# Performance work log

Measured on AMD Instinct MI355X. Metric: run time of the kernel, lower is better.

## Reference

```python
import jax, jax.numpy as jnp
import numpy as np

N_HEADS = 16
NEG = -1e9  # matches torch masked_fill value


def setup_inputs() -> dict:
    key = jax.random.key(0)
    ks = jax.random.split(key, 8)
    B, S, E = 4, 1024, 1024
    x = jax.random.normal(ks[0], (B, S, E), dtype=jnp.float32)
    event_lengths = jax.random.randint(ks[1], (B,), 1, S + 1)
    scale = 1.0 / np.sqrt(E)
    Wq = jax.random.normal(ks[2], (E, E), dtype=jnp.float32) * scale
    bq = jnp.zeros((E,), dtype=jnp.float32)
    Wk = jax.random.normal(ks[3], (E, E), dtype=jnp.float32) * scale
    bk = jnp.zeros((E,), dtype=jnp.float32)
    Wv = jax.random.normal(ks[4], (E, E), dtype=jnp.float32) * scale
    bv = jnp.zeros((E,), dtype=jnp.float32)
    return {"x": x, "Wq": Wq, "bq": bq, "Wk": Wk, "bk": bk,
            "Wv": Wv, "bv": bv, "event_lengths": event_lengths}


def reference(x, Wq, bq, Wk, bk, Wv, bv, event_lengths):
    B, S, E = x.shape
    H = N_HEADS
    D = E // H
    # fused projections, then split heads: [B,S,E] -> [B,H,S,D]
    def split(t):
        return t.reshape(B, S, H, D).transpose(0, 2, 1, 3)
    q = split(x @ Wq + bq)
    k = split(x @ Wk + bk)
    v = split(x @ Wv + bv)
    scores = jnp.einsum('bhsd,bhtd->bhst', q, k) / jnp.sqrt(jnp.float32(D))
    # rectangular length mask: valid iff row < len AND col < len
    idx = jnp.arange(S)
    valid = idx[None, :] < event_lengths[:, None]           # [B,S]
    mask = valid[:, :, None] & valid[:, None, :]            # [B,S,S]
    scores = jnp.where(mask[:, None, :, :], scores, NEG)
    attn = jax.nn.softmax(scores, axis=-1)
    out = jnp.einsum('bhst,bhtd->bhsd', attn, v)            # [B,H,S,D]
    # concat heads (== torch.cat over head outputs); NOTE: summarize proj is
    # dead code in the original (its result is overwritten), dropout is eval-identity
    return out.transpose(0, 2, 1, 3).reshape(B, S, E)
```

## Files before the change

kernel.cpp:

```cpp
#include <hip/hip_runtime.h>
#include <stdint.h>


using u16     = unsigned short;
using half8   = __attribute__((ext_vector_type(8))) _Float16;
using floatx4 = __attribute__((ext_vector_type(4))) float;

#define MFMA16(a, b, c) __builtin_amdgcn_mfma_f32_16x16x32_f16(a, b, c, 0, 0, 0)

__device__ __forceinline__ u16 f2h(float f) {
  _Float16 h = (_Float16)f; u16 u; __builtin_memcpy(&u, &h, 2); return u;
}

template <int CTRL>
__device__ __forceinline__ float dppf(float v) {
  return __int_as_float(__builtin_amdgcn_update_dpp(
      0, __float_as_int(v), CTRL, 0xF, 0xF, true));
}
__device__ __forceinline__ float rowsum16(float v) {
  v += dppf<0x121>(v);
  v += dppf<0x122>(v);
  v += dppf<0x124>(v);
  v += dppf<0x128>(v);
  return v;
}

__device__ __forceinline__ void async_cp16(void* lds, const void* g) {
  __builtin_amdgcn_global_load_lds(
      (__attribute__((address_space(1))) uint32_t*)(uintptr_t)g,
      (__attribute__((address_space(3))) uint32_t*)(uint32_t)(uintptr_t)lds,
      16, 0, 0);
}

__global__ void k_prep(const float* __restrict__ x, u16* __restrict__ xh,
                       const float* __restrict__ w0, const float* __restrict__ w1,
                       const float* __restrict__ w2,
                       u16* __restrict__ o0, u16* __restrict__ o1,
                       u16* __restrict__ o2, float* __restrict__ vsum) {
  __shared__ float t[32][33];
  const int bx = blockIdx.x;
  if (bx < 4096) {
    int i = (bx * 256 + threadIdx.x) * 4;
    float4 v = *(const float4*)(x + i);
    ushort4 hv;
    hv.x = f2h(v.x);
    hv.y = f2h(v.y);
    hv.z = f2h(v.z);
    hv.w = f2h(v.w);
    *(ushort4*)(xh + i) = hv;
    if (bx == 0) {
      float4 z = {0.f, 0.f, 0.f, 0.f};
#pragma unroll
      for (int e = 0; e < 4; e++) ((float4*)vsum)[threadIdx.x * 4 + e] = z;
    }
    return;
  }
  const int id = bx - 4096;
  const int z = id >> 10, rem = id & 1023;
  const float* W = z == 0 ? w0 : (z == 1 ? w1 : w2);
  u16* oh = z == 0 ? o0 : (z == 1 ? o1 : o2);
  const int kb = (rem & 31) * 32, nb = (rem >> 5) * 32;
  const int tx = threadIdx.x & 31, ty = threadIdx.x >> 5;
  for (int r = ty; r < 32; r += 8) t[r][tx] = W[(kb + r) * 1024 + nb + tx];
  __syncthreads();
  for (int r = ty; r < 32; r += 8)
    oh[(nb + r) * 1024 + kb + tx] = f2h(t[tx][r]);
}

__launch_bounds__(256, 4)
__global__ void k_proj(const u16* __restrict__ xh,
                       const u16* __restrict__ wqT, const u16* __restrict__ wkT,
                       const u16* __restrict__ wvT,
                       const float* __restrict__ bq, const float* __restrict__ bk,
                       const float* __restrict__ bv,
                       u16* __restrict__ qh, u16* __restrict__ kh,
                       u16* __restrict__ vth, float* __restrict__ vsum) {
  __shared__ u16 Sm[17408];
  const int z = blockIdx.z;
  const u16* wT = z == 0 ? wqT : (z == 1 ? wkT : wvT);
  const float* bias = z == 0 ? bq : (z == 1 ? bk : bv);
  u16* oh = z == 0 ? qh : (z == 1 ? kh : vth);
  const float oscale = (z == 0) ? 0.18033688011112042f : 1.0f;

  const int tid = threadIdx.x, l = tid & 63, w = tid >> 6;
  const int quad = l >> 4, col = l & 15;
  const int m0 = blockIdx.x * 128, n0 = blockIdx.y * 128;
  const int wm = (w & 1) * 64, wn = (w >> 1) * 64;

  const int row0 = tid >> 3, ch = tid & 7;
  const int sc8 = (ch ^ (row0 & 7)) * 8;
  int gofs[4], lofs[4];
#pragma unroll
  for (int p = 0; p < 4; p++) {
    gofs[p] = (row0 + 32 * p) * 1024 + sc8;
    lofs[p] = (tid + p * 256) * 8;
  }

  const u16* Ag = xh + m0 * 1024;
  const u16* Bg = wT + n0 * 1024;

  int ar[2][4], br[2][4];
#pragma unroll
  for (int ks = 0; ks < 2; ks++) {
#pragma unroll
    for (int i = 0; i < 4; i++) {
      int r = wm + i * 16 + col;
      ar[ks][i] = r * 64 + (((ks * 4 + quad) ^ (r & 7)) * 8);
    }
#pragma unroll
    for (int j = 0; j < 4; j++) {
      int r = wn + j * 16 + col;
      br[ks][j] = r * 64 + (((ks * 4 + quad) ^ (r & 7)) * 8);
    }
  }

  floatx4 zero4 = {0.f, 0.f, 0.f, 0.f};
  floatx4 acc[4][4];
#pragma unroll
  for (int i = 0; i < 4; i++)
#pragma unroll
    for (int j = 0; j < 4; j++) acc[i][j] = zero4;

  for (int k0 = 0; k0 < 1024; k0 += 64) {
    __syncthreads();
#pragma unroll
    for (int p = 0; p < 4; p++) async_cp16(Sm + lofs[p], Ag + gofs[p] + k0);
#pragma unroll
    for (int p = 0; p < 4; p++)
      async_cp16(Sm + 8192 + lofs[p], Bg + gofs[p] + k0);
    __syncthreads();

#pragma unroll
    for (int ks = 0; ks < 2; ks++) {
      half8 fa[4], fb[4];
#pragma unroll
      for (int i = 0; i < 4; i++) fa[i] = *(const half8*)(Sm + ar[ks][i]);
#pragma unroll
      for (int j = 0; j < 4; j++)
        fb[j] = *(const half8*)(Sm + 8192 + br[ks][j]);
#pragma unroll
      for (int i = 0; i < 4; i++)
#pragma unroll
        for (int j = 0; j < 4; j++) acc[i][j] = MFMA16(fa[i], fb[j], acc[i][j]);
    }
  }

  const int bidx = m0 >> 10;
  const int sbase = m0 & 1023;
  __syncthreads();

#pragma unroll
  for (int j = 0; j < 4; j++) {
    int nloc = wn + j * 16 + col;
    float bb = bias[n0 + nloc];
#pragma unroll
    for (int i = 0; i < 4; i++)
#pragma unroll
      for (int r = 0; r < 4; r++) {
        int mloc = wm + i * 16 + quad * 4 + r;
        Sm[mloc * 136 + nloc] = f2h((acc[i][j][r] + bb) * oscale);
      }
  }
  __syncthreads();

  if (z != 2) {
#pragma unroll
    for (int k = 0; k < 8; k++) {
      int c = tid + k * 256;
      int mloc = c >> 4, n = (c & 15) * 8;
      int hh = (n0 + n) >> 6, d = (n0 + n) & 63;
      half8 vv = *(const half8*)(Sm + mloc * 136 + n);
      *(half8*)(oh + ((bidx * 16 + hh) * 1024 + sbase + mloc) * 64 + d) = vv;
    }
  } else {
#pragma unroll
    for (int k = 0; k < 8; k++) {
      int c = tid + k * 256;
      int nloc = c & 127, s0 = (c >> 7) * 8;
      int hh = (n0 + nloc) >> 6, d = (n0 + nloc) & 63;
      u16 tmp[8];
#pragma unroll
      for (int e = 0; e < 8; e++) tmp[e] = Sm[(s0 + e) * 136 + nloc];
      *(half8*)(vth + ((bidx * 16 + hh) * 64 + d) * 1024 + sbase + s0) =
          *(half8*)tmp;
    }
#pragma unroll
    for (int j = 0; j < 4; j++) {
      int nloc = wn + j * 16 + col;
      float bb = bias[n0 + nloc];
      float part = 16.0f * bb;
#pragma unroll
      for (int i = 0; i < 4; i++)
#pragma unroll
        for (int r = 0; r < 4; r++) part += acc[i][j][r];
      part += __shfl_xor(part, 16, 64);
      part += __shfl_xor(part, 32, 64);
      if (quad == 0) {
        int hh = (n0 + nloc) >> 6, d = (n0 + nloc) & 63;
        unsafeAtomicAdd(vsum + (bidx * 16 + hh) * 64 + d, part);
      }
    }
  }
}

__device__ __forceinline__ void stage64(u16* lds, const u16* g, int row_stride,
                                        int tid) {
#pragma unroll
  for (int p = 0; p < 2; p++) {
    int slot = (p * 256 + tid) * 8;
    int row = slot >> 6;
    int gp = (slot >> 3) & 7;
    int gl = gp ^ (row & 7);
    async_cp16(lds + slot, g + row * row_stride + gl * 8);
  }
}

__launch_bounds__(256)
__global__ void k_attn(const u16* __restrict__ qh_g,
                       const u16* __restrict__ kh_g,
                       const u16* __restrict__ vth_g,
                       const float* __restrict__ vsum, const int* __restrict__ elen,
                       float* __restrict__ out) {
  __shared__ u16 QP[4096];
  __shared__ u16 Bufs[2][8192];
  const int tid = threadIdx.x, l = tid & 63, w = tid >> 6;
  const int quad = l >> 4, col = l & 15;
  const int id = blockIdx.x;
  const int b = (id + (id >> 8)) & 3;
  const int h = (id >> 2) & 15;
  const int bh = b * 16 + h;
  const int q0 = ((id >> 6) & 15) * 64;
  const int len = elen[b];

  if (q0 >= len) {
    float val = vsum[bh * 64 + l] * (1.0f / 1024.0f);
    float* op = out + (b * 1024 + q0) * 1024 + h * 64 + l;
    for (int r = w; r < 64; r += 4) op[r * 1024] = val;
    return;
  }

  const u16* kh_b  = kh_g + bh * 65536;
  const u16* vth_b = vth_g + bh * 65536;

  stage64(QP, qh_g + (bh * 1024 + q0) * 64, 64, tid);
  stage64(Bufs[0], kh_b, 64, tid);
  stage64(Bufs[0] + 4096, vth_b, 1024, tid);
  __syncthreads();

  half8 qf[2];
  {
    int qrow = w * 16 + col;
#pragma unroll
    for (int ks = 0; ks < 2; ks++)
      qf[ks] = *(const half8*)(QP + qrow * 64 +
                               (((ks * 4 + quad) ^ (qrow & 7)) * 8));
  }

  int kvo[2][4];
#pragma unroll
  for (int ks = 0; ks < 2; ks++)
#pragma unroll
    for (int j = 0; j < 4; j++) {
      int n = j * 16 + col;
      kvo[ks][j] = n * 64 + (((ks * 4 + quad) ^ (n & 7)) * 8);
    }
  int p_rd[2];
#pragma unroll
  for (int ks = 0; ks < 2; ks++) {
    int row = w * 16 + col;
    p_rd[ks] = row * 64 + (((ks * 4 + quad) ^ (row & 7)) * 8);
  }
  int p_wr[4][4];
#pragma unroll
  for (int r = 0; r < 4; r++) {
    int row = w * 16 + quad * 4 + r;
#pragma unroll
    for (int j = 0; j < 4; j++) {
      int cj = j * 2 + (col >> 3);
      p_wr[r][j] = row * 64 + ((cj ^ (row & 7)) * 8) + (col & 7);
    }
  }

  floatx4 zero4 = {0.f, 0.f, 0.f, 0.f};
  floatx4 O[4];
  float lp[4];
#pragma unroll
  for (int j = 0; j < 4; j++) O[j] = zero4;
#pragma unroll
  for (int r = 0; r < 4; r++) lp[r] = 0.f;

  const int ntt = (len + 63) >> 6;
  for (int tt = 0; tt < ntt; ++tt) {
    const int t0 = tt * 64;
    u16* cur = Bufs[tt & 1];
    if (tt + 1 < ntt) {
      u16* nxt = Bufs[(tt + 1) & 1];
      const int t1 = t0 + 64;
      stage64(nxt, kh_b + t1 * 64, 64, tid);
      stage64(nxt + 4096, vth_b + t1, 1024, tid);
    }

    floatx4 sc[4];
#pragma unroll
    for (int j = 0; j < 4; j++) sc[j] = zero4;
#pragma unroll
    for (int ks = 0; ks < 2; ks++) {
#pragma unroll
      for (int j = 0; j < 4; j++) {
        half8 kb = *(const half8*)(cur + kvo[ks][j]);
        sc[j] = MFMA16(qf[ks], kb, sc[j]);
      }
    }

    if (t0 + 64 > len) {
#pragma unroll
      for (int j = 0; j < 4; j++) {
        bool inv = (t0 + j * 16 + col) >= len;
#pragma unroll
        for (int r = 0; r < 4; r++)
          if (inv) sc[j][r] = -3e38f;
      }
    }

#pragma unroll
    for (int r = 0; r < 4; r++) {
#pragma unroll
      for (int j = 0; j < 4; j++) {
        float e = __builtin_exp2f(sc[j][r]);
        QP[p_wr[r][j]] = f2h(e);
        lp[r] += e;
      }
    }

#pragma unroll
    for (int ks = 0; ks < 2; ks++) {
      half8 pa = *(const half8*)(QP + p_rd[ks]);
#pragma unroll
      for (int j = 0; j < 4; j++) {
        half8 vb = *(const half8*)(cur + 4096 + kvo[ks][j]);
        O[j] = MFMA16(pa, vb, O[j]);
      }
    }

    __syncthreads();
  }

  float l_r[4];
#pragma unroll
  for (int r = 0; r < 4; r++) l_r[r] = rowsum16(lp[r]);
#pragma unroll
  for (int r = 0; r < 4; r++) {
    int s = q0 + w * 16 + quad * 4 + r;
    float invl = 1.0f / l_r[r];
    bool valid = (s < len);
#pragma unroll
    for (int j = 0; j < 4; j++) {
      int d = j * 16 + col;
      float val = valid ? O[j][r] * invl : vsum[bh * 64 + d] * (1.0f / 1024.0f);
      out[(b * 1024 + s) * 1024 + h * 64 + d] = val;
    }
  }
}

extern "C" void kernel_launch(void* const* d_in, const int* in_sizes, int n_in,
                              void* d_out, int out_size, void* d_ws, size_t ws_size,
                              hipStream_t stream) {
  (void)in_sizes; (void)n_in; (void)out_size; (void)ws_size;
  const float* x  = (const float*)d_in[0];
  const float* Wq = (const float*)d_in[1];
  const float* bq = (const float*)d_in[2];
  const float* Wk = (const float*)d_in[3];
  const float* bk = (const float*)d_in[4];
  const float* Wv = (const float*)d_in[5];
  const float* bv = (const float*)d_in[6];
  const int* elen = (const int*)d_in[7];
  float* out = (float*)d_out;

  char* ws = (char*)d_ws;
  const size_t MB = 1024 * 1024;
  u16* xh  = (u16*)(ws + 0 * MB);
  u16* wqT = (u16*)(ws + 8 * MB);
  u16* wkT = (u16*)(ws + 10 * MB);
  u16* wvT = (u16*)(ws + 12 * MB);
  u16* qh  = (u16*)(ws + 14 * MB);
  u16* kh  = (u16*)(ws + 22 * MB);
  u16* vth = (u16*)(ws + 30 * MB);
  float* vsum = (float*)(ws + 38 * MB);

  k_prep<<<7168, 256, 0, stream>>>(x, xh, Wq, Wk, Wv, wqT, wkT, wvT, vsum);
  k_proj<<<dim3(32, 8, 3), 256, 0, stream>>>(xh, wqT, wkT, wvT, bq, bk, bv,
                                             qh, kh, vth, vsum);
  k_attn<<<1024, 256, 0, stream>>>(qh, kh, vth, vsum, elen, out);
}
```

Baseline: 150.2 us.

## Process 128 query rows per attention block to reuse K/V tiles

Each attention block now handles two 64-row query groups instead of one, halving the grid to 512 blocks. Each staged K/V tile is reused for twice as many query rows, cutting global K/V traffic and staging work per output row. The cost is more registers per thread (two accumulator sets, preloaded K fragments), more LDS, and fewer blocks to spread across the GPU. Length-skewed batches could also leave work less evenly balanced.

```diff
diff --git a/kernel.cpp b/kernel.cpp
--- a/kernel.cpp
+++ b/kernel.cpp
@@ -221,7 +221,7 @@
                        const u16* __restrict__ vth_g,
                        const float* __restrict__ vsum, const int* __restrict__ elen,
                        float* __restrict__ out) {
-  __shared__ u16 QP[4096];
+  __shared__ u16 QP[8192];
   __shared__ u16 Bufs[2][8192];
   const int tid = threadIdx.x, l = tid & 63, w = tid >> 6;
   const int quad = l >> 4, col = l & 15;
@@ -229,13 +229,13 @@
   const int b = (id + (id >> 8)) & 3;
   const int h = (id >> 2) & 15;
   const int bh = b * 16 + h;
-  const int q0 = ((id >> 6) & 15) * 64;
+  const int q0 = ((id >> 6) & 7) * 128;
   const int len = elen[b];
 
   if (q0 >= len) {
     float val = vsum[bh * 64 + l] * (1.0f / 1024.0f);
     float* op = out + (b * 1024 + q0) * 1024 + h * 64 + l;
-    for (int r = w; r < 64; r += 4) op[r * 1024] = val;
+    for (int r = w; r < 128; r += 4) op[r * 1024] = val;
     return;
   }
 
@@ -243,17 +243,21 @@
   const u16* vth_b = vth_g + bh * 65536;
 
   stage64(QP, qh_g + (bh * 1024 + q0) * 64, 64, tid);
+  stage64(QP + 4096, qh_g + (bh * 1024 + q0 + 64) * 64, 64, tid);
   stage64(Bufs[0], kh_b, 64, tid);
   stage64(Bufs[0] + 4096, vth_b, 1024, tid);
   __syncthreads();
 
-  half8 qf[2];
+  half8 qf[2][2];
   {
     int qrow = w * 16 + col;
-#pragma unroll
-    for (int ks = 0; ks < 2; ks++)
-      qf[ks] = *(const half8*)(QP + qrow * 64 +
-                               (((ks * 4 + quad) ^ (qrow & 7)) * 8));
+    int base = qrow * 64;
+#pragma unroll
+    for (int ks = 0; ks < 2; ks++) {
+      int o = (((ks * 4 + quad) ^ (qrow & 7)) * 8);
+      qf[0][ks] = *(const half8*)(QP + base + o);
+      qf[1][ks] = *(const half8*)(QP + 4096 + base + o);
+    }
   }
 
   int kvo[2][4];
@@ -282,12 +286,15 @@
   }
 
   floatx4 zero4 = {0.f, 0.f, 0.f, 0.f};
-  floatx4 O[4];
-  float lp[4];
-#pragma unroll
-  for (int j = 0; j < 4; j++) O[j] = zero4;
-#pragma unroll
-  for (int r = 0; r < 4; r++) lp[r] = 0.f;
+  floatx4 O[2][4];
+  float lp[2][4];
+#pragma unroll
+  for (int g = 0; g < 2; g++) {
+#pragma unroll
+    for (int j = 0; j < 4; j++) O[g][j] = zero4;
+#pragma unroll
+    for (int r = 0; r < 4; r++) lp[g][r] = 0.f;
+  }
 
   const int ntt = (len + 63) >> 6;
   for (int tt = 0; tt < ntt; ++tt) {
@@ -300,64 +307,79 @@
       stage64(nxt + 4096, vth_b + t1, 1024, tid);
     }
 
-    floatx4 sc[4];
-#pragma unroll
-    for (int j = 0; j < 4; j++) sc[j] = zero4;
+    half8 kb[2][4];
+#pragma unroll
+    for (int ks = 0; ks < 2; ks++)
+#pragma unroll
+      for (int j = 0; j < 4; j++)
+        kb[ks][j] = *(const half8*)(cur + kvo[ks][j]);
+
+    const bool tail = (t0 + 64 > len);
+#pragma unroll
+    for (int g = 0; g < 2; g++) {
+      floatx4 sc[4];
+#pragma unroll
+      for (int j = 0; j < 4; j++) sc[j] = zero4;
+#pragma unroll
+      for (int ks = 0; ks < 2; ks++)
+#pragma unroll
+        for (int j = 0; j < 4; j++)
+          sc[j] = MFMA16(qf[g][ks], kb[ks][j], sc[j]);
+
+      if (tail) {
+#pragma unroll
+        for (int j = 0; j < 4; j++) {
+          bool inv = (t0 + j * 16 + col) >= len;
+#pragma unroll
+          for (int r = 0; r < 4; r++)
+            if (inv) sc[j][r] = -3e38f;
+        }
+      }
+
+#pragma unroll
+      for (int r = 0; r < 4; r++) {
+#pragma unroll
+        for (int j = 0; j < 4; j++) {
+          float e = __builtin_exp2f(sc[j][r]);
+          QP[g * 4096 + p_wr[r][j]] = f2h(e);
+          lp[g][r] += e;
+        }
+      }
+    }
+
 #pragma unroll
     for (int ks = 0; ks < 2; ks++) {
+      half8 vb[4];
+#pragma unroll
+      for (int j = 0; j < 4; j++)
+        vb[j] = *(const half8*)(cur + 4096 + kvo[ks][j]);
+      half8 pa0 = *(const half8*)(QP + p_rd[ks]);
+      half8 pa1 = *(const half8*)(QP + 4096 + p_rd[ks]);
 #pragma unroll
       for (int j = 0; j < 4; j++) {
-        half8 kb = *(const half8*)(cur + kvo[ks][j]);
-        sc[j] = MFMA16(qf[ks], kb, sc[j]);
-      }
-    }
-
-    if (t0 + 64 > len) {
+        O[0][j] = MFMA16(pa0, vb[j], O[0][j]);
+        O[1][j] = MFMA16(pa1, vb[j], O[1][j]);
+      }
+    }
+
+    __syncthreads();
+  }
+
+#pragma unroll
+  for (int g = 0; g < 2; g++) {
+#pragma unroll
+    for (int r = 0; r < 4; r++) {
+      float l_r = rowsum16(lp[g][r]);
+      int s = q0 + g * 64 + w * 16 + quad * 4 + r;
+      float invl = 1.0f / l_r;
+      bool valid = (s < len);
 #pragma unroll
       for (int j = 0; j < 4; j++) {
-        bool inv = (t0 + j * 16 + col) >= len;
-#pragma unroll
-        for (int r = 0; r < 4; r++)
-          if (inv) sc[j][r] = -3e38f;
-      }
-    }
-
-#pragma unroll
-    for (int r = 0; r < 4; r++) {
-#pragma unroll
-      for (int j = 0; j < 4; j++) {
-        float e = __builtin_exp2f(sc[j][r]);
-        QP[p_wr[r][j]] = f2h(e);
-        lp[r] += e;
-      }
-    }
-
-#pragma unroll
-    for (int ks = 0; ks < 2; ks++) {
-      half8 pa = *(const half8*)(QP + p_rd[ks]);
-#pragma unroll
-      for (int j = 0; j < 4; j++) {
-        half8 vb = *(const half8*)(cur + 4096 + kvo[ks][j]);
-        O[j] = MFMA16(pa, vb, O[j]);
-      }
-    }
-
-    __syncthreads();
-  }
-
-  float l_r[4];
-#pragma unroll
-  for (int r = 0; r < 4; r++) l_r[r] = rowsum16(lp[r]);
-#pragma unroll
-  for (int r = 0; r < 4; r++) {
-    int s = q0 + w * 16 + quad * 4 + r;
-    float invl = 1.0f / l_r[r];
-    bool valid = (s < len);
-#pragma unroll
-    for (int j = 0; j < 4; j++) {
-      int d = j * 16 + col;
-      float val = valid ? O[j][r] * invl : vsum[bh * 64 + d] * (1.0f / 1024.0f);
-      out[(b * 1024 + s) * 1024 + h * 64 + d] = val;
+        int d = j * 16 + col;
+        float val = valid ? O[g][j][r] * invl
+                          : vsum[bh * 64 + d] * (1.0f / 1024.0f);
+        out[(b * 1024 + s) * 1024 + h * 64 + d] = val;
+      }
     }
   }
 }
@@ -390,5 +412,5 @@
   k_prep<<<7168, 256, 0, stream>>>(x, xh, Wq, Wk, Wv, wqT, wkT, wvT, vsum);
   k_proj<<<dim3(32, 8, 3), 256, 0, stream>>>(xh, wqT, wkT, wvT, bq, bk, bv,
                                              qh, kh, vth, vsum);
-  k_attn<<<1024, 256, 0, stream>>>(qh, kh, vth, vsum, elen, out);
-}
+  k_attn<<<512, 256, 0, stream>>>(qh, kh, vth, vsum, elen, out);
+}
```

Measured after the change: 152.0 us. Within noise of the previous version (+1.2%).

## Load K/V tiles directly from global into registers, drop LDS staging and barriers

Applied to the files above, without the earlier changes.

Replaces the double-buffered async LDS staging of K and V tiles with direct per-lane global loads of MFMA fragments into registers. The P tile now goes to a small per-wave padded LDS region, so the block-wide __syncthreads per tile is removed. Less LDS and no barrier could raise occupancy and cut sync overhead. The cost is that each wave re-reads K/V from global/L2 with no cross-wave sharing and no explicit prefetch, so latency is exposed and register pressure rises.

```diff
diff --git a/kernel.cpp b/kernel.cpp
--- a/kernel.cpp
+++ b/kernel.cpp
@@ -203,26 +203,13 @@
   }
 }
 
-__device__ __forceinline__ void stage64(u16* lds, const u16* g, int row_stride,
-                                        int tid) {
-#pragma unroll
-  for (int p = 0; p < 2; p++) {
-    int slot = (p * 256 + tid) * 8;
-    int row = slot >> 6;
-    int gp = (slot >> 3) & 7;
-    int gl = gp ^ (row & 7);
-    async_cp16(lds + slot, g + row * row_stride + gl * 8);
-  }
-}
-
 __launch_bounds__(256)
 __global__ void k_attn(const u16* __restrict__ qh_g,
                        const u16* __restrict__ kh_g,
                        const u16* __restrict__ vth_g,
                        const float* __restrict__ vsum, const int* __restrict__ elen,
                        float* __restrict__ out) {
-  __shared__ u16 QP[4096];
-  __shared__ u16 Bufs[2][8192];
+  __shared__ u16 P[4 * 1280];
   const int tid = threadIdx.x, l = tid & 63, w = tid >> 6;
   const int quad = l >> 4, col = l & 15;
   const int id = blockIdx.x;
@@ -239,47 +226,19 @@
     return;
   }
 
-  const u16* kh_b  = kh_g + bh * 65536;
-  const u16* vth_b = vth_g + bh * 65536;
-
-  stage64(QP, qh_g + (bh * 1024 + q0) * 64, 64, tid);
-  stage64(Bufs[0], kh_b, 64, tid);
-  stage64(Bufs[0] + 4096, vth_b, 1024, tid);
-  __syncthreads();
-
   half8 qf[2];
   {
-    int qrow = w * 16 + col;
-#pragma unroll
-    for (int ks = 0; ks < 2; ks++)
-      qf[ks] = *(const half8*)(QP + qrow * 64 +
-                               (((ks * 4 + quad) ^ (qrow & 7)) * 8));
-  }
-
-  int kvo[2][4];
-#pragma unroll
-  for (int ks = 0; ks < 2; ks++)
-#pragma unroll
-    for (int j = 0; j < 4; j++) {
-      int n = j * 16 + col;
-      kvo[ks][j] = n * 64 + (((ks * 4 + quad) ^ (n & 7)) * 8);
-    }
-  int p_rd[2];
-#pragma unroll
-  for (int ks = 0; ks < 2; ks++) {
-    int row = w * 16 + col;
-    p_rd[ks] = row * 64 + (((ks * 4 + quad) ^ (row & 7)) * 8);
-  }
-  int p_wr[4][4];
-#pragma unroll
-  for (int r = 0; r < 4; r++) {
-    int row = w * 16 + quad * 4 + r;
-#pragma unroll
-    for (int j = 0; j < 4; j++) {
-      int cj = j * 2 + (col >> 3);
-      p_wr[r][j] = row * 64 + ((cj ^ (row & 7)) * 8) + (col & 7);
-    }
-  }
+    const u16* qb = qh_g + (bh * 1024 + q0 + w * 16 + col) * 64 + quad * 8;
+    qf[0] = *(const half8*)(qb);
+    qf[1] = *(const half8*)(qb + 32);
+  }
+
+  const u16* kb_g = kh_g + bh * 65536;
+  const u16* vb_g = vth_g + bh * 65536;
+
+  u16* Pw = P + w * 1280;
+  const int p_rd0 = col * 72 + quad * 8;
+  const int p_wb = (quad * 4) * 72 + col;
 
   floatx4 zero4 = {0.f, 0.f, 0.f, 0.f};
   floatx4 O[4];
@@ -292,25 +251,31 @@
   const int ntt = (len + 63) >> 6;
   for (int tt = 0; tt < ntt; ++tt) {
     const int t0 = tt * 64;
-    u16* cur = Bufs[tt & 1];
-    if (tt + 1 < ntt) {
-      u16* nxt = Bufs[(tt + 1) & 1];
-      const int t1 = t0 + 64;
-      stage64(nxt, kh_b + t1 * 64, 64, tid);
-      stage64(nxt + 4096, vth_b + t1, 1024, tid);
-    }
+
+    half8 kb[2][4];
+#pragma unroll
+    for (int ks = 0; ks < 2; ks++)
+#pragma unroll
+      for (int j = 0; j < 4; j++)
+        kb[ks][j] = *(const half8*)(kb_g + (t0 + j * 16 + col) * 64 +
+                                    ks * 32 + quad * 8);
 
     floatx4 sc[4];
 #pragma unroll
     for (int j = 0; j < 4; j++) sc[j] = zero4;
 #pragma unroll
-    for (int ks = 0; ks < 2; ks++) {
-#pragma unroll
-      for (int j = 0; j < 4; j++) {
-        half8 kb = *(const half8*)(cur + kvo[ks][j]);
-        sc[j] = MFMA16(qf[ks], kb, sc[j]);
-      }
-    }
+    for (int ks = 0; ks < 2; ks++)
+#pragma unroll
+      for (int j = 0; j < 4; j++)
+        sc[j] = MFMA16(qf[ks], kb[ks][j], sc[j]);
+
+    half8 vb[2][4];
+#pragma unroll
+    for (int ks = 0; ks < 2; ks++)
+#pragma unroll
+      for (int j = 0; j < 4; j++)
+        vb[ks][j] = *(const half8*)(vb_g + (j * 16 + col) * 1024 + t0 +
+                                    ks * 32 + quad * 8);
 
     if (t0 + 64 > len) {
 #pragma unroll
@@ -327,22 +292,18 @@
 #pragma unroll
       for (int j = 0; j < 4; j++) {
         float e = __builtin_exp2f(sc[j][r]);
-        QP[p_wr[r][j]] = f2h(e);
+        Pw[p_wb + r * 72 + j * 16] = f2h(e);
         lp[r] += e;
       }
     }
 
 #pragma unroll
     for (int ks = 0; ks < 2; ks++) {
-      half8 pa = *(const half8*)(QP + p_rd[ks]);
-#pragma unroll
-      for (int j = 0; j < 4; j++) {
-        half8 vb = *(const half8*)(cur + 4096 + kvo[ks][j]);
-        O[j] = MFMA16(pa, vb, O[j]);
-      }
-    }
-
-    __syncthreads();
+      half8 pa = *(const half8*)(Pw + p_rd0 + ks * 32);
+#pragma unroll
+      for (int j = 0; j < 4; j++)
+        O[j] = MFMA16(pa, vb[ks][j], O[j]);
+    }
   }
 
   float l_r[4];
```

After: 213.0 us. +41.8%, slower.
